# Kernel optimization log

Hardware: AMD Instinct MI355X
Metric: run time of the kernel (lower is better)

## Reference

```python
import jax, jax.numpy as jnp
import numpy as np

B, T, NQ, NT = 64, 256, 32, 32
NR = NQ - 1          # queries 1..31 are matched (query 0 = ego)
BIG = jnp.float32(1e6)   # cost for invalid (padded) target columns
W_CLASS, W_POS, W_VEL = 1.0, 5.0, 2.0


def setup_inputs() -> dict:
    key = jax.random.key(0)
    k1, k2, k3, k4, k5 = jax.random.split(key, 5)
    position = jax.random.normal(k1, (B, T, NQ, 3), jnp.float32)
    velocity = jax.random.normal(k2, (B, T, NQ, 3), jnp.float32)
    class_logits = jax.random.normal(k3, (B, T, NQ, 5), jnp.float32)
    targets = jax.random.normal(k4, (B, T, NT, 18), jnp.float32)
    # raw: 0 = invalid (all-zero onehot), 1 = ego (onehot idx 0), 2..4 -> onehot idx 1..3
    raw = jax.random.randint(k5, (B, T, NT), 0, 5)
    onehot = jnp.where(raw[..., None] > 0,
                       jax.nn.one_hot(jnp.maximum(raw - 1, 0), 4, dtype=jnp.float32),
                       0.0)
    targets = targets.at[..., 14:18].set(onehot)
    return {"position": position, "velocity": velocity,
            "class_logits": class_logits, "targets": targets}


def _cost_and_valid(position, velocity, class_logits, targets):
    # drop ego query 0
    pred_pos = position[:, :, 1:, :]          # [B,T,NR,3]
    pred_vel = velocity[:, :, 1:, :]
    probs = jax.nn.softmax(class_logits[:, :, 1:, :], axis=-1)   # [B,T,NR,5]
    tgt_pos = targets[..., 0:3]               # [B,T,NT,3]
    tgt_vel = targets[..., 3:6]
    oh = targets[..., 14:18]
    s = oh.sum(-1)
    idx4 = jnp.argmax(oh, -1)
    cls5 = jnp.where(s == 0, 0, idx4 + 1)     # [B,T,NT], 5-way class index
    valid = (s > 0) & (cls5 != 1)             # drop empty + ego targets
    # cost_class[b,t,q,j] = -probs[b,t,q,cls5[b,t,j]]
    cls_ix = jnp.broadcast_to(cls5[:, :, None, :, None], (B, T, NR, NT, 1))
    cost_cls = -jnp.take_along_axis(probs[:, :, :, None, :], cls_ix, axis=-1)[..., 0]
    cost_pos = jnp.abs(pred_pos[:, :, :, None, :] - tgt_pos[:, :, None, :, :]).sum(-1)
    cost_vel = jnp.abs(pred_vel[:, :, :, None, :] - tgt_vel[:, :, None, :, :]).sum(-1)
    C = W_CLASS * cost_cls + W_POS * cost_pos + W_VEL * cost_vel   # [B,T,NR,NT]
    return C, valid


def _lap(cost):
    # Jonker-Volgenant / Hungarian shortest augmenting path (e-maxx formulation),
    # rectangular n <= m. cost: [n, m]. Returns row2col [n] int32.
    n, m = cost.shape
    INF = jnp.float32(1e18)
    a = jnp.zeros((n + 1, m + 1), jnp.float32).at[1:, 1:].set(cost)  # 1-indexed
    cols = jnp.arange(m + 1, dtype=jnp.int32)

    def outer(i, uvp):
        u, v, p = uvp                      # potentials + p[j] = row matched to col j
        p = p.at[0].set(i)
        st = (u, v, p, jnp.full(m + 1, INF), jnp.zeros(m + 1, bool),
              jnp.zeros(m + 1, jnp.int32), jnp.int32(0))

        def cond(st):
            return st[2][st[6]] != 0

        def body(st):
            u, v, p, minv, used, way, j0 = st
            used = used.at[j0].set(True)
            i0 = p[j0]
            cur = a[i0] - u[i0] - v                       # reduced costs, [m+1]
            upd = (~used) & (cols > 0) & (cur < minv)
            minv = jnp.where(upd, cur, minv)
            way = jnp.where(upd, j0, way)
            cand = jnp.where(used | (cols == 0), INF, minv)
            j1 = jnp.argmin(cand).astype(jnp.int32)
            delta = cand[j1]
            u = u.at[p].add(jnp.where(used, delta, 0.0))
            v = v - jnp.where(used, delta, 0.0)
            minv = jnp.where(used, minv, minv - delta)
            return (u, v, p, minv, used, way, j1)

        u, v, p, _, _, way, j0 = jax.lax.while_loop(cond, body, st)

        def aug_body(s):
            p, j0 = s
            j1 = way[j0]
            return p.at[j0].set(p[j1]), j1

        p, _ = jax.lax.while_loop(lambda s: s[1] != 0, aug_body, (p, j0))
        return (u, v, p)

    u0 = jnp.zeros(n + 1, jnp.float32)
    v0 = jnp.zeros(m + 1, jnp.float32)
    p0 = jnp.zeros(m + 1, jnp.int32)
    _, _, p = jax.lax.fori_loop(1, n + 1, lambda i, c: outer(jnp.int32(i), c), (u0, v0, p0))
    # invert: p[j] = row -> row2col[row] = j (skip virtual col 0; free cols map to dummy row 0)
    row2col = jnp.zeros(n + 1, jnp.int32).at[p[1:]].set(cols[1:])
    return row2col[1:] - 1                                # 0-based col per row


@jax.jit
def _forward(position, velocity, class_logits, targets):
    C, valid = _cost_and_valid(position, velocity, class_logits, targets)
    # invalid target columns padded with a constant BIG cost; since it is constant
    # per column the optimal sub-assignment on valid columns equals scipy's
    # linear_sum_assignment on the valid-only rectangular matrix.
    Cm = jnp.where(valid[:, :, None, :], C, BIG)
    row2col = jax.vmap(_lap)(Cm.reshape(-1, NR, NT)).reshape(B, T, NR)  # [B,T,NR]
    assigned_valid = jnp.take_along_axis(valid, row2col, axis=-1)       # [B,T,NR]
    pred_idx = jnp.where(assigned_valid, jnp.arange(1, NQ, dtype=jnp.int32), -1)
    tgt_idx = jnp.where(assigned_valid, row2col, -1)
    return C, pred_idx, tgt_idx


def reference(position, velocity, class_logits, targets):
    # Returns (cost tensor [B,T,NR,NT], pred_idx [B,T,NR], tgt_idx [B,T,NR]).
    # (pred_idx[b,t,k], tgt_idx[b,t,k]) with pred_idx != -1 are the matched pairs,
    # equivalent to the original's per-frame (pred_indices, target_indices) lists.
    return _forward(position, velocity, class_logits, targets)
```

## Files before the change

kernel.cpp:

```cpp
#include <hip/hip_runtime.h>
#include <cmath>

#define NPROB 16384
#define PROBS_PER_BLOCK 4

template<int CTRL>
__device__ __forceinline__ float fmin_dpp(float x) {
  int s = __builtin_amdgcn_update_dpp(0, __float_as_int(x), CTRL, 0xF, 0xF, true);
  return fminf(x, __int_as_float(s));
}

__device__ __forceinline__ float halfmin32(float x) {
  x = fmin_dpp<0xB1>(x);
  x = fmin_dpp<0x4E>(x);
  x = fmin_dpp<0x141>(x);
  x = fmin_dpp<0x140>(x);
  int s = __builtin_amdgcn_ds_swizzle(__float_as_int(x), 0x401F);
  return fminf(x, __int_as_float(s));
}

__device__ __forceinline__ int bperm_i(int addr, int v) {
  return __builtin_amdgcn_ds_bpermute(addr, v);
}
__device__ __forceinline__ float bperm_f(int addr, float v) {
  return __int_as_float(__builtin_amdgcn_ds_bpermute(addr, __float_as_int(v)));
}

__global__ __launch_bounds__(128, 5) void matcher_kernel(
    const float* __restrict__ position,
    const float* __restrict__ velocity,
    const float* __restrict__ logits,
    const float* __restrict__ targets,
    float* __restrict__ out)
{
#pragma clang fp contract(off)
  __shared__ float sCm[PROBS_PER_BLOCK][992];
  __shared__ int   sR2c[PROBS_PER_BLOCK][32];

  const int tid  = threadIdx.x;
  const int lane = tid & 63;
  const int rel  = lane & 31;
  const int hs   = lane & 32;
  const int hs4  = hs * 4;
  const int relp1 = rel + 1;
  const int lp   = tid >> 5;
  const int bt   = blockIdx.x * PROBS_PER_BLOCK + lp;

  const float* pos = position + (size_t)bt * 96;
  const float* vel = velocity + (size_t)bt * 96;
  const float* lg  = logits   + (size_t)bt * 160;
  const float* tg  = targets  + (size_t)bt * 576;

  const float* trow = tg + rel * 18;
  const float tp0 = trow[0],  tp1 = trow[1],  tp2 = trow[2];
  const float tv0 = trow[3],  tv1 = trow[4],  tv2 = trow[5];
  const float o0  = trow[14], o1  = trow[15], o2  = trow[16], o3 = trow[17];
  const float ssum = ((o0 + o1) + o2) + o3;
  const float mxo  = fmaxf(fmaxf(fmaxf(o0, o1), o2), o3);
  const int idx4 = (o0 == mxo) ? 0 : ((o1 == mxo) ? 1 : ((o2 == mxo) ? 2 : 3));
  const int cls5 = (ssum == 0.0f) ? 0 : (idx4 + 1);
  const int validc = (ssum > 0.0f && cls5 != 1) ? 1 : 0;

  float m_l = 0.0f, s_l = 1.0f;
  if (rel < 31) {
    const float* lr = lg + (rel + 1) * 5;
    const float l0 = lr[0], l1 = lr[1], l2 = lr[2], l3 = lr[3], l4 = lr[4];
    m_l = fmaxf(fmaxf(fmaxf(fmaxf(l0, l1), l2), l3), l4);
    const float e0 = expf(l0 - m_l), e1 = expf(l1 - m_l), e2 = expf(l2 - m_l),
                e3 = expf(l3 - m_l), e4 = expf(l4 - m_l);
    s_l = (((e0 + e1) + e2) + e3) + e4;
  }

  float* outC  = out + (size_t)bt * 992;
  float* cmrow = &sCm[lp][0];
  for (int r = 0; r < 31; ++r) {
    const float m_r = __shfl(m_l, hs + r, 64);
    const float s_r = __shfl(s_l, hs + r, 64);
    const float lgl = lg[(r + 1) * 5 + cls5];
    const float psel = expf(lgl - m_r) / s_r;
    const float pr0 = pos[(r + 1) * 3 + 0], pr1 = pos[(r + 1) * 3 + 1], pr2 = pos[(r + 1) * 3 + 2];
    const float vr0 = vel[(r + 1) * 3 + 0], vr1 = vel[(r + 1) * 3 + 1], vr2 = vel[(r + 1) * 3 + 2];
    const float cp = (fabsf(pr0 - tp0) + fabsf(pr1 - tp1)) + fabsf(pr2 - tp2);
    const float cv = (fabsf(vr0 - tv0) + fabsf(vr1 - tv1)) + fabsf(vr2 - tv2);
    const float Cv = (-psel + 5.0f * cp) + 2.0f * cv;
    outC[r * 32 + rel]  = Cv;
    cmrow[r * 32 + rel] = validc ? Cv : 1000000.0f;
  }

  const float INF = 1e18f;
  float u = 0.0f;
  float v = 0.0f;
  int   p = 0;

  const float* cmb = cmrow + rel - 32;

  for (int i = 1; i <= 31; ++i) {
    float uq = bperm_f(hs4 + 4 * p - 4, u);
    const float u_i = __shfl(u, hs + (i - 1), 64);

    float rowf = (rel == i - 1) ? 1.0f : 0.0f;
    int   way  = -1;

    float mv = (cmb[i * 32] - u_i) - v;
    const float mval = halfmin32(mv);
    unsigned mh = (unsigned)(__ballot(mv == mval) >> hs);
    int j0 = (int)__builtin_ctz(mh);
    u = fmaf(rowf, mval, u);
    mv -= mval;
    int   pj = bperm_i(hs4 + 4 * j0, p);
    float u0 = bperm_f(hs4 + 4 * j0, uq);

    while (pj != 0) {
      mv = (rel == j0) ? INF : mv;
      const bool um = (mv == INF);
      rowf = (relp1 == pj) ? 1.0f : rowf;
      const float a2 = cmb[pj * 32];
      const float c2 = um ? INF : ((a2 - u0) - v);
      if (c2 < mv) { mv = c2; way = j0; }
      const float mv2 = halfmin32(mv);
      mh = (unsigned)(__ballot(mv == mv2) >> hs);
      j0 = (int)__builtin_ctz(mh);
      const float dv = um ? mv2 : 0.0f;
      u = fmaf(rowf, mv2, u);
      v -= dv;
      uq += dv;
      mv -= mv2;
      pj = bperm_i(hs4 + 4 * j0, p);
      u0 = bperm_f(hs4 + 4 * j0, uq);
    }

    while (true) {
      const int w1 = __shfl(way, hs + j0, 64);
      const int pv = __shfl(p, hs + ((w1 < 0) ? 0 : w1), 64);
      const int pja = (w1 < 0) ? i : pv;
      if (rel == j0) p = pja;
      if (w1 < 0) break;
      j0 = w1;
    }
  }

  if (p > 0) sR2c[lp][p - 1] = rel;
  const int col  = sR2c[lp][rel & 31];
  const int colc = col & 31;
  const int av   = __shfl(validc, hs + colc, 64);
  if (rel < 31) {
    const size_t base1 = (size_t)NPROB * 992;
    const size_t base2 = base1 + (size_t)NPROB * 31;
    out[base1 + (size_t)bt * 31 + rel] = av ? (float)(rel + 1) : -1.0f;
    out[base2 + (size_t)bt * 31 + rel] = av ? (float)col : -1.0f;
  }
}

extern "C" void kernel_launch(void* const* d_in, const int* in_sizes, int n_in,
                              void* d_out, int out_size, void* d_ws, size_t ws_size,
                              hipStream_t stream) {
  const float* position = (const float*)d_in[0];
  const float* velocity = (const float*)d_in[1];
  const float* logits   = (const float*)d_in[2];
  const float* targets  = (const float*)d_in[3];
  float* out = (float*)d_out;
  matcher_kernel<<<NPROB / PROBS_PER_BLOCK, 128, 0, stream>>>(
      position, velocity, logits, targets, out);
}
```

Measured before the change: 382.8 us.

## Use persistent blocks with atomic work-stealing over problem pairs

Replaces the one-block-per-four-problems launch with a fixed persistent grid. Each wavefront repeatedly grabs a pair of assignment problems from a global atomic counter, which is zeroed with a memset before launch. The aim is to balance the variable-length Hungarian solves across wavefronts and reduce tail imbalance. It also replaces the per-column uq dual update with a sticky 'used' flag, and it adds an atomic per pair, a memset, and a dependence on the workspace pointer.

```diff
diff --git a/kernel.cpp b/kernel.cpp
--- a/kernel.cpp
+++ b/kernel.cpp
@@ -2,7 +2,9 @@
 #include <cmath>
 
 #define NPROB 16384
+#define NPAIRS (NPROB / 2)
 #define PROBS_PER_BLOCK 4
+#define GRID_BLOCKS 2560
 
 template<int CTRL>
 __device__ __forceinline__ float fmin_dpp(float x) {
@@ -31,7 +33,8 @@
     const float* __restrict__ velocity,
     const float* __restrict__ logits,
     const float* __restrict__ targets,
-    float* __restrict__ out)
+    float* __restrict__ out,
+    int* __restrict__ gctr)
 {
 #pragma clang fp contract(off)
   __shared__ float sCm[PROBS_PER_BLOCK][992];
@@ -43,111 +46,120 @@
   const int hs   = lane & 32;
   const int hs4  = hs * 4;
   const int relp1 = rel + 1;
-  const int lp   = tid >> 5;
-  const int bt   = blockIdx.x * PROBS_PER_BLOCK + lp;
+  const int wv   = tid >> 6;
+  const int lp   = wv * 2 + (hs >> 5);
 
-  const float* pos = position + (size_t)bt * 96;
-  const float* vel = velocity + (size_t)bt * 96;
-  const float* lg  = logits   + (size_t)bt * 160;
-  const float* tg  = targets  + (size_t)bt * 576;
-
-  const float* trow = tg + rel * 18;
-  const float tp0 = trow[0],  tp1 = trow[1],  tp2 = trow[2];
-  const float tv0 = trow[3],  tv1 = trow[4],  tv2 = trow[5];
-  const float o0  = trow[14], o1  = trow[15], o2  = trow[16], o3 = trow[17];
-  const float ssum = ((o0 + o1) + o2) + o3;
-  const float mxo  = fmaxf(fmaxf(fmaxf(o0, o1), o2), o3);
-  const int idx4 = (o0 == mxo) ? 0 : ((o1 == mxo) ? 1 : ((o2 == mxo) ? 2 : 3));
-  const int cls5 = (ssum == 0.0f) ? 0 : (idx4 + 1);
-  const int validc = (ssum > 0.0f && cls5 != 1) ? 1 : 0;
-
-  float m_l = 0.0f, s_l = 1.0f;
-  if (rel < 31) {
-    const float* lr = lg + (rel + 1) * 5;
-    const float l0 = lr[0], l1 = lr[1], l2 = lr[2], l3 = lr[3], l4 = lr[4];
-    m_l = fmaxf(fmaxf(fmaxf(fmaxf(l0, l1), l2), l3), l4);
-    const float e0 = expf(l0 - m_l), e1 = expf(l1 - m_l), e2 = expf(l2 - m_l),
-                e3 = expf(l3 - m_l), e4 = expf(l4 - m_l);
-    s_l = (((e0 + e1) + e2) + e3) + e4;
-  }
-
-  float* outC  = out + (size_t)bt * 992;
   float* cmrow = &sCm[lp][0];
-  for (int r = 0; r < 31; ++r) {
-    const float m_r = __shfl(m_l, hs + r, 64);
-    const float s_r = __shfl(s_l, hs + r, 64);
-    const float lgl = lg[(r + 1) * 5 + cls5];
-    const float psel = expf(lgl - m_r) / s_r;
-    const float pr0 = pos[(r + 1) * 3 + 0], pr1 = pos[(r + 1) * 3 + 1], pr2 = pos[(r + 1) * 3 + 2];
-    const float vr0 = vel[(r + 1) * 3 + 0], vr1 = vel[(r + 1) * 3 + 1], vr2 = vel[(r + 1) * 3 + 2];
-    const float cp = (fabsf(pr0 - tp0) + fabsf(pr1 - tp1)) + fabsf(pr2 - tp2);
-    const float cv = (fabsf(vr0 - tv0) + fabsf(vr1 - tv1)) + fabsf(vr2 - tv2);
-    const float Cv = (-psel + 5.0f * cp) + 2.0f * cv;
-    outC[r * 32 + rel]  = Cv;
-    cmrow[r * 32 + rel] = validc ? Cv : 1000000.0f;
-  }
-
-  const float INF = 1e18f;
-  float u = 0.0f;
-  float v = 0.0f;
-  int   p = 0;
-
   const float* cmb = cmrow + rel - 32;
 
-  for (int i = 1; i <= 31; ++i) {
-    float uq = bperm_f(hs4 + 4 * p - 4, u);
-    const float u_i = __shfl(u, hs + (i - 1), 64);
+  for (;;) {
+    int pr = 0;
+    if (lane == 0) pr = atomicAdd(gctr, 1);
+    pr = __shfl(pr, 0, 64);
+    if (pr >= NPAIRS) break;
+    const int bt = pr * 2 + (hs >> 5);
 
-    float rowf = (rel == i - 1) ? 1.0f : 0.0f;
-    int   way  = -1;
+    const float* pos = position + (size_t)bt * 96;
+    const float* vel = velocity + (size_t)bt * 96;
+    const float* lg  = logits   + (size_t)bt * 160;
+    const float* tg  = targets  + (size_t)bt * 576;
 
-    float mv = (cmb[i * 32] - u_i) - v;
-    const float mval = halfmin32(mv);
-    unsigned mh = (unsigned)(__ballot(mv == mval) >> hs);
-    int j0 = (int)__builtin_ctz(mh);
-    u = fmaf(rowf, mval, u);
-    mv -= mval;
-    int   pj = bperm_i(hs4 + 4 * j0, p);
-    float u0 = bperm_f(hs4 + 4 * j0, uq);
+    const float* trow = tg + rel * 18;
+    const float tp0 = trow[0],  tp1 = trow[1],  tp2 = trow[2];
+    const float tv0 = trow[3],  tv1 = trow[4],  tv2 = trow[5];
+    const float o0  = trow[14], o1  = trow[15], o2  = trow[16], o3 = trow[17];
+    const float ssum = ((o0 + o1) + o2) + o3;
+    const float mxo  = fmaxf(fmaxf(fmaxf(o0, o1), o2), o3);
+    const int idx4 = (o0 == mxo) ? 0 : ((o1 == mxo) ? 1 : ((o2 == mxo) ? 2 : 3));
+    const int cls5 = (ssum == 0.0f) ? 0 : (idx4 + 1);
+    const int validc = (ssum > 0.0f && cls5 != 1) ? 1 : 0;
 
-    while (pj != 0) {
-      mv = (rel == j0) ? INF : mv;
-      const bool um = (mv == INF);
-      rowf = (relp1 == pj) ? 1.0f : rowf;
-      const float a2 = cmb[pj * 32];
-      const float c2 = um ? INF : ((a2 - u0) - v);
-      if (c2 < mv) { mv = c2; way = j0; }
-      const float mv2 = halfmin32(mv);
-      mh = (unsigned)(__ballot(mv == mv2) >> hs);
-      j0 = (int)__builtin_ctz(mh);
-      const float dv = um ? mv2 : 0.0f;
-      u = fmaf(rowf, mv2, u);
-      v -= dv;
-      uq += dv;
-      mv -= mv2;
-      pj = bperm_i(hs4 + 4 * j0, p);
-      u0 = bperm_f(hs4 + 4 * j0, uq);
+    float m_l = 0.0f, s_l = 1.0f;
+    if (rel < 31) {
+      const float* lr = lg + (rel + 1) * 5;
+      const float l0 = lr[0], l1 = lr[1], l2 = lr[2], l3 = lr[3], l4 = lr[4];
+      m_l = fmaxf(fmaxf(fmaxf(fmaxf(l0, l1), l2), l3), l4);
+      const float e0 = expf(l0 - m_l), e1 = expf(l1 - m_l), e2 = expf(l2 - m_l),
+                  e3 = expf(l3 - m_l), e4 = expf(l4 - m_l);
+      s_l = (((e0 + e1) + e2) + e3) + e4;
     }
 
-    while (true) {
-      const int w1 = __shfl(way, hs + j0, 64);
-      const int pv = __shfl(p, hs + ((w1 < 0) ? 0 : w1), 64);
-      const int pja = (w1 < 0) ? i : pv;
-      if (rel == j0) p = pja;
-      if (w1 < 0) break;
-      j0 = w1;
+    float* outC = out + (size_t)bt * 992;
+    for (int r = 0; r < 31; ++r) {
+      const float m_r = __shfl(m_l, hs + r, 64);
+      const float s_r = __shfl(s_l, hs + r, 64);
+      const float lgl = lg[(r + 1) * 5 + cls5];
+      const float psel = expf(lgl - m_r) / s_r;
+      const float pr0 = pos[(r + 1) * 3 + 0], pr1 = pos[(r + 1) * 3 + 1], pr2 = pos[(r + 1) * 3 + 2];
+      const float vr0 = vel[(r + 1) * 3 + 0], vr1 = vel[(r + 1) * 3 + 1], vr2 = vel[(r + 1) * 3 + 2];
+      const float cp = (fabsf(pr0 - tp0) + fabsf(pr1 - tp1)) + fabsf(pr2 - tp2);
+      const float cv = (fabsf(vr0 - tv0) + fabsf(vr1 - tv1)) + fabsf(vr2 - tv2);
+      const float Cv = (-psel + 5.0f * cp) + 2.0f * cv;
+      outC[r * 32 + rel]  = Cv;
+      cmrow[r * 32 + rel] = validc ? Cv : 1000000.0f;
     }
-  }
 
-  if (p > 0) sR2c[lp][p - 1] = rel;
-  const int col  = sR2c[lp][rel & 31];
-  const int colc = col & 31;
-  const int av   = __shfl(validc, hs + colc, 64);
-  if (rel < 31) {
-    const size_t base1 = (size_t)NPROB * 992;
-    const size_t base2 = base1 + (size_t)NPROB * 31;
-    out[base1 + (size_t)bt * 31 + rel] = av ? (float)(rel + 1) : -1.0f;
-    out[base2 + (size_t)bt * 31 + rel] = av ? (float)col : -1.0f;
+    const float INF = 1e18f;
+    float u = 0.0f;
+    float v = 0.0f;
+    int   p = 0;
+
+    for (int i = 1; i <= 31; ++i) {
+      const float uq = bperm_f(hs4 + 4 * p - 4, u);
+      const float u_i = __shfl(u, hs + (i - 1), 64);
+
+      bool  used = false;
+      float rowf = (rel == i - 1) ? 1.0f : 0.0f;
+      int   way  = -1;
+
+      float mv = (cmb[i * 32] - u_i) - v;
+      const float mval = halfmin32(mv);
+      unsigned mh = (unsigned)(__ballot(mv == mval) >> hs);
+      int j0 = (int)__builtin_ctz(mh);
+      u = fmaf(rowf, mval, u);
+      mv -= mval;
+      int   pj = bperm_i(hs4 + 4 * j0, p);
+      float u0 = bperm_f(hs4 + 4 * j0, uq);
+
+      while (pj != 0) {
+        const bool pop = (rel == j0);
+        used = used || pop;
+        mv = pop ? INF : mv;
+        rowf = (relp1 == pj) ? 1.0f : rowf;
+        const float a2 = cmb[pj * 32];
+        const float c2 = used ? INF : ((a2 - u0) - v);
+        if (c2 < mv) { mv = c2; way = j0; }
+        const float mv2 = halfmin32(mv);
+        mh = (unsigned)(__ballot(mv == mv2) >> hs);
+        j0 = (int)__builtin_ctz(mh);
+        const float dv = used ? mv2 : 0.0f;
+        u = fmaf(rowf, mv2, u);
+        v -= dv;
+        mv -= mv2;
+        pj = bperm_i(hs4 + 4 * j0, p);
+        u0 = bperm_f(hs4 + 4 * j0, uq);
+      }
+
+      while (true) {
+        const int w1 = __shfl(way, hs + j0, 64);
+        const int pv = __shfl(p, hs + ((w1 < 0) ? 0 : w1), 64);
+        const int pja = (w1 < 0) ? i : pv;
+        if (rel == j0) p = pja;
+        if (w1 < 0) break;
+        j0 = w1;
+      }
+    }
+
+    if (p > 0) sR2c[lp][p - 1] = rel;
+    const int col  = sR2c[lp][rel & 31];
+    const int colc = col & 31;
+    const int av   = __shfl(validc, hs + colc, 64);
+    if (rel < 31) {
+      const size_t base1 = (size_t)NPROB * 992;
+      const size_t base2 = base1 + (size_t)NPROB * 31;
+      out[base1 + (size_t)bt * 31 + rel] = av ? (float)(rel + 1) : -1.0f;
+      out[base2 + (size_t)bt * 31 + rel] = av ? (float)col : -1.0f;
+    }
   }
 }
 
@@ -159,6 +171,8 @@
   const float* logits   = (const float*)d_in[2];
   const float* targets  = (const float*)d_in[3];
   float* out = (float*)d_out;
-  matcher_kernel<<<NPROB / PROBS_PER_BLOCK, 128, 0, stream>>>(
-      position, velocity, logits, targets, out);
+  int* gctr = (int*)d_ws;
+  hipMemsetAsync(gctr, 0, sizeof(int), stream);
+  matcher_kernel<<<GRID_BLOCKS, 128, 0, stream>>>(
+      position, velocity, logits, targets, out, gctr);
 }
```

New measurement: 423.3 us. 1.11x slower.
